# Performance work log

Measured on AMD Instinct MI355X. Metric: run time of the kernel, lower is better.

The kernel has to match this reference:

```python
import jax, jax.numpy as jnp
import numpy as np

IN_FEATURES = 256
OUT_FEATURES = 256
INTERNAL = (IN_FEATURES + OUT_FEATURES) // 2  # trajectron AdditiveAttention default


def setup_inputs() -> dict:
    key = jax.random.key(0)
    k1, k2, k3, k4, k5 = jax.random.split(key, 5)
    B, TH, TQ = 32, 256, 64
    inputs = jax.random.normal(k1, (B, TH, IN_FEATURES), dtype=jnp.float32)
    state = jax.random.normal(k2, (B, TQ, OUT_FEATURES), dtype=jnp.float32)
    # Linear weights (no bias), Kaiming-ish scale
    w1 = jax.random.normal(k3, (INTERNAL, IN_FEATURES), dtype=jnp.float32) / np.sqrt(IN_FEATURES)
    w2 = jax.random.normal(k4, (INTERNAL, OUT_FEATURES), dtype=jnp.float32) / np.sqrt(OUT_FEATURES)
    v = jax.random.normal(k5, (INTERNAL,), dtype=jnp.float32) / np.sqrt(INTERNAL)
    return {"inputs": inputs, "state": state, "w1": w1, "w2": w2, "v": v, "batch_size": B}


def reference(inputs, state, w1, w2, v, batch_size):
    # history annotations: (B, Th, Din); future annotations (queries): (B, Tq, Dout)
    keys = inputs.reshape(batch_size, -1, IN_FEATURES)
    queries = state.reshape(batch_size, -1, OUT_FEATURES)
    # Additive (Bahdanau) attention: score = v . tanh(W1 k + W2 q)
    k_proj = jnp.einsum('bti,di->btd', keys, w1)       # (B, Th, D)
    q_proj = jnp.einsum('bqo,do->bqd', queries, w2)    # (B, Tq, D)
    scores = jnp.einsum('d,bqtd->bqt', v, jnp.tanh(q_proj[:, :, None, :] + k_proj[:, None, :, :]))
    alpha = jax.nn.softmax(scores, axis=-1)            # softmax over history axis
    contexts = jnp.einsum('bqt,bti->bqi', alpha, keys)  # (B, Tq, Din)
    # reshape + dropout (eval mode / p effectively 0 -> identity)
    return contexts.reshape(-1, IN_FEATURES)
```

## Files before the change

### kernel.cpp

```cpp
#include <hip/hip_runtime.h>
#include <math.h>

#define BATCH 32
#define TH    256
#define TQn   64
#define DIN   256
#define DD    256
#define QT    4
#define E2C   2.885390081777927f
#define NL2E  -2.8853900817779268f

typedef __attribute__((ext_vector_type(8)))  short bf16x8;
typedef __attribute__((ext_vector_type(16))) float floatx16;
typedef __attribute__((ext_vector_type(4)))  float f32x4;
typedef __attribute__((ext_vector_type(2)))  float f32x2;

__device__ __forceinline__ float eclamp(float x) {
    return __builtin_amdgcn_exp2f(fminf(x * E2C, 15.f));
}

__device__ __forceinline__ f32x2 pk_fma_s(f32x2 a, f32x2 b, f32x2 c) {
    f32x2 d;
    asm("v_pk_fma_f32 %0, %1, %2, %3" : "=v"(d) : "s"(a), "v"(b), "v"(c));
    return d;
}
__device__ __forceinline__ f32x2 pk_mul_s(f32x2 a, f32x2 b) {
    f32x2 d;
    asm("v_pk_mul_f32 %0, %1, %2" : "=v"(d) : "s"(a), "v"(b));
    return d;
}
__device__ __forceinline__ f32x2 pk_mul_v(f32x2 a, f32x2 b) {
    f32x2 d;
    asm("v_pk_mul_f32 %0, %1, %2" : "=v"(d) : "v"(a), "v"(b));
    return d;
}

__device__ __forceinline__ unsigned cvt_pk_bf16(float x0, float x1) {
    unsigned r;
    asm("v_cvt_pk_bf16_f32 %0, %1, %2" : "=v"(r) : "v"(x0), "v"(x1));
    return r;
}
__device__ __forceinline__ void split2(float x0, float x1, unsigned& hi, unsigned& lo) {
    unsigned h = cvt_pk_bf16(x0, x1);
    float f0 = __uint_as_float(h << 16);
    float f1 = __uint_as_float(h & 0xFFFF0000u);
    hi = h;
    lo = cvt_pk_bf16(x0 - f0, x1 - f1);
}

__device__ __forceinline__ void split8(float4 f0, float4 f1, uint4& hi, uint4& lo) {
    split2(f0.x, f0.y, hi.x, lo.x);
    split2(f0.z, f0.w, hi.y, lo.y);
    split2(f1.x, f1.y, hi.z, lo.z);
    split2(f1.z, f1.w, hi.w, lo.w);
}

#define REG4  65
#define WOFF  (16 * REG4)
#define TSTR  68
__global__ __launch_bounds__(256, 4)
void proj_kernel(const float* __restrict__ keys,
                 const float* __restrict__ state,
                 const float* __restrict__ w1,
                 const float* __restrict__ w2,
                 const float* __restrict__ vvec,
                 float* __restrict__ ktp,
                 float* __restrict__ qpo,
                 float* __restrict__ vperm)
{
    __shared__ uint4 lds4[2 * 16 * REG4];

    const int bid = blockIdx.x;
    const int tid = threadIdx.x;

    const int xcd  = bid & 7;
    const int slot = bid >> 3;
    const int bb   = xcd + 8 * (slot / 20);
    const int j    = slot % 20;

    const float* X;
    const float* W;
    int m0, n0;
    bool is_kp;
    if (j < 16) {
        is_kp = true;
        m0 = bb * 256 + (j >> 2) * 64;
        n0 = (j & 3) * 64;
        X = keys; W = w1;
    } else {
        is_kp = false;
        m0 = bb * 64;
        n0 = (j - 16) * 64;
        X = state; W = w2;
    }

    const int w    = tid >> 6;
    const int l    = tid & 63;
    const int mt   = w >> 1;
    const int nt   = w & 1;
    const int srow = tid >> 3;
    const int kg   = tid & 7;
    const int s_s  = kg >> 1;
    const int lidx = (srow & 31) + 32 * (kg & 1);

    floatx16 acc = {};

    #pragma unroll
    for (int k0 = 0; k0 < DIN; k0 += 64) {
        #pragma unroll
        for (int hrow = 0; hrow < 2; hrow++) {
            int m = srow + hrow * 32;
            const float* px = X + (size_t)(m0 + m) * DIN + k0 + kg * 8;
            uint4 hi, lo;
            split8(*(const float4*)px, *(const float4*)(px + 4), hi, lo);
            int g = m >> 5;
            lds4[((0 * 2 + g) * 4 + s_s) * REG4 + lidx] = hi;
            lds4[((2 + g) * 4 + s_s) * REG4 + lidx] = lo;
            const float* pw = W + (size_t)(n0 + m) * DIN + k0 + kg * 8;
            split8(*(const float4*)pw, *(const float4*)(pw + 4), hi, lo);
            lds4[WOFF + ((0 * 2 + g) * 4 + s_s) * REG4 + lidx] = hi;
            lds4[WOFF + ((2 + g) * 4 + s_s) * REG4 + lidx] = lo;
        }
        __syncthreads();

        #pragma unroll
        for (int s = 0; s < 4; s++) {
            uint4 ahr = lds4[((0 * 2 + mt) * 4 + s) * REG4 + l];
            uint4 alr = lds4[((2 + mt) * 4 + s) * REG4 + l];
            uint4 bhr = lds4[WOFF + ((0 * 2 + nt) * 4 + s) * REG4 + l];
            uint4 blr = lds4[WOFF + ((2 + nt) * 4 + s) * REG4 + l];
            bf16x8 ah = __builtin_bit_cast(bf16x8, ahr);
            bf16x8 al = __builtin_bit_cast(bf16x8, alr);
            bf16x8 bh = __builtin_bit_cast(bf16x8, bhr);
            bf16x8 bl = __builtin_bit_cast(bf16x8, blr);
            acc = __builtin_amdgcn_mfma_f32_32x32x16_bf16(ah, bh, acc, 0, 0, 0);
            acc = __builtin_amdgcn_mfma_f32_32x32x16_bf16(al, bh, acc, 0, 0, 0);
            acc = __builtin_amdgcn_mfma_f32_32x32x16_bf16(ah, bl, acc, 0, 0, 0);
        }
        __syncthreads();
    }

    const int col = l & 31;
    const int hl  = l >> 5;
    if (is_kp) {
        float* sT = (float*)lds4;
        const int d_local = nt * 32 + col;
        #pragma unroll
        for (int r = 0; r < 16; r++) {
            int t_local = mt * 32 + 4 * hl + 8 * (r >> 2) + (r & 3);
            sT[t_local * TSTR + d_local] = eclamp(acc[r]);
        }
        __syncthreads();
        const int b  = m0 >> 8;
        const int t0 = m0 & 255;
        float4* dst4 = (float4*)ktp;
        #pragma unroll
        for (int p = 0; p < 4; p++) {
            int dp_local = w * 4 + p;
            float4 v4 = *(float4*)&sT[l * TSTR + dp_local * 4];
            float4 w4;
            w4.x = v4.x; w4.y = v4.z; w4.z = v4.y; w4.w = v4.w;
            dst4[(size_t)(b * 64 + (n0 >> 2) + dp_local) * 256 + t0 + l] = w4;
        }
    } else {
        const int d  = n0 + nt * 32 + col;
        const int dl = d & 3;
        const int dsd = (d & ~3) | ((dl & 1) << 1) | (dl >> 1);
        #pragma unroll
        for (int r = 0; r < 16; r++) {
            int row = (r & 3) + 8 * (r >> 2) + 4 * hl;
            qpo[(size_t)(m0 + mt * 32 + row) * DD + dsd] = eclamp(acc[r]);
        }
        if (!is_kp && bb == 0 && n0 == 0 && tid < 256) {
            int jl = tid & 3;
            vperm[tid] = vvec[(tid & ~3) | ((jl & 1) << 1) | (jl >> 1)];
        }
    }
}

__global__ __launch_bounds__(1024, 8)
void attn_kernel(const float* __restrict__ keys,
                 const float* __restrict__ vvec,
                 const float* __restrict__ ktp,
                 const float* __restrict__ qp,
                 float* __restrict__ out)
{
    __shared__ float s_part[4][QT][TH];
    __shared__ float s_alpha[QT][TH];
    __shared__ float s_rsum[QT];

    const int bid  = blockIdx.x;
    const int b    = bid & 31;
    const int q0   = (bid >> 5) * QT;
    const int tid  = threadIdx.x;
    const int t    = tid & 255;
    const int dgu  = __builtin_amdgcn_readfirstlane(tid >> 8);
    const int lane = tid & 63;
    const int wv   = tid >> 6;

    float acc[QT];
    #pragma unroll
    for (int q = 0; q < QT; q++) acc[q] = 0.f;

    const float4* kb4 = (const float4*)ktp + ((size_t)(b * 64 + dgu * 16) * 256 + t);
    const float* pqr0 = qp + (size_t)(b * TQn + q0 + 0) * DD + dgu * 64;
    const float* pqr1 = qp + (size_t)(b * TQn + q0 + 1) * DD + dgu * 64;
    const float* pqr2 = qp + (size_t)(b * TQn + q0 + 2) * DD + dgu * 64;
    const float* pqr3 = qp + (size_t)(b * TQn + q0 + 3) * DD + dgu * 64;
    const float* vvp  = vvec + dgu * 64;

    const f32x2 one2 = {1.f, 1.f};

    float4 kv0 = kb4[0 * 256], kv1 = kb4[1 * 256],
           kv2 = kb4[2 * 256], kv3 = kb4[3 * 256];

    #pragma unroll
    for (int c = 0; c < 4; c++) {
        float4 n0v, n1v, n2v, n3v;
        if (c < 3) {
            const float4* p = kb4 + (size_t)(c + 1) * 4 * 256;
            n0v = p[0 * 256]; n1v = p[1 * 256];
            n2v = p[2 * 256]; n3v = p[3 * 256];
        }
        #pragma unroll
        for (int u = 0; u < 4; u++) {
            const int dp = c * 4 + u;
            float4 kv = (u == 0) ? kv0 : (u == 1) ? kv1 : (u == 2) ? kv2 : kv3;
            f32x2 KA = {kv.x, kv.y};
            f32x2 KB = {kv.z, kv.w};
            f32x4 V4 = *(const f32x4*)(vvp + dp * 4);
            f32x2 VA = {V4[0], V4[1]};
            f32x2 VB = {V4[2], V4[3]};
            const float* pqr[QT] = {pqr0, pqr1, pqr2, pqr3};
            #pragma unroll
            for (int q = 0; q < QT; q++) {
                const float* pr = pqr[q];
                f32x4 P4 = *(const f32x4*)(pr + dp * 4);
                f32x2 PA = {P4[0], P4[1]};
                f32x2 PB = {P4[2], P4[3]};
                f32x2 A = pk_fma_s(PA, KA, one2);
                f32x2 B = pk_fma_s(PB, KB, one2);
                f32x2 D = pk_mul_v(A, B);
                f32x2 T = pk_mul_s(VA, B);
                f32x2 N = pk_fma_s(VB, A, T);
                float num = fmaf(N[1], D[0], N[0] * D[1]);
                float den = D[0] * D[1];
                acc[q] = fmaf(num, __builtin_amdgcn_rcpf(den), acc[q]);
            }
        }
        if (c < 3) { kv0 = n0v; kv1 = n1v; kv2 = n2v; kv3 = n3v; }
    }

    #pragma unroll
    for (int q = 0; q < QT; q++) s_part[dgu][q][t] = acc[q];
    __syncthreads();

    if (wv < QT) {
        const int q = wv;
        float p0 = s_part[0][q][lane]       + s_part[1][q][lane]
                 + s_part[2][q][lane]       + s_part[3][q][lane];
        float p1 = s_part[0][q][lane + 64]  + s_part[1][q][lane + 64]
                 + s_part[2][q][lane + 64]  + s_part[3][q][lane + 64];
        float p2 = s_part[0][q][lane + 128] + s_part[1][q][lane + 128]
                 + s_part[2][q][lane + 128] + s_part[3][q][lane + 128];
        float p3 = s_part[0][q][lane + 192] + s_part[1][q][lane + 192]
                 + s_part[2][q][lane + 192] + s_part[3][q][lane + 192];
        float e0 = __builtin_amdgcn_exp2f(p0 * NL2E);
        float e1 = __builtin_amdgcn_exp2f(p1 * NL2E);
        float e2 = __builtin_amdgcn_exp2f(p2 * NL2E);
        float e3 = __builtin_amdgcn_exp2f(p3 * NL2E);
        s_alpha[q][lane]       = e0;
        s_alpha[q][lane + 64]  = e1;
        s_alpha[q][lane + 128] = e2;
        s_alpha[q][lane + 192] = e3;
        float s = (e0 + e1) + (e2 + e3);
        #pragma unroll
        for (int off = 32; off >= 1; off >>= 1) s += __shfl_xor(s, off);
        if (lane == 0) s_rsum[q] = 1.f / s;
    }
    __syncthreads();

    {
        const int iqg = __builtin_amdgcn_readfirstlane((tid >> 6) & 3);
        const int il  = lane & 15;
        const int tl  = lane >> 4;
        const int iq  = iqg * 16 + il;

        f32x4 ctx4[QT] = {};
        const float* kp0 = keys + ((size_t)b * TH + dgu * 64 + tl) * DIN + iq * 4;

        #pragma unroll 4
        for (int step = 0; step < 16; step++) {
            f32x4 key4 = *(const f32x4*)(kp0 + (size_t)step * 4 * DIN);
            const int ta = dgu * 64 + step * 4 + tl;
            #pragma unroll
            for (int q = 0; q < QT; q++)
                ctx4[q] += key4 * s_alpha[q][ta];
        }

        #pragma unroll
        for (int q = 0; q < QT; q++) {
            #pragma unroll
            for (int k = 0; k < 4; k++) {
                ctx4[q][k] += __shfl_xor(ctx4[q][k], 16);
                ctx4[q][k] += __shfl_xor(ctx4[q][k], 32);
            }
        }
        if (tl == 0) {
            #pragma unroll
            for (int q = 0; q < QT; q++)
                *(f32x4*)&s_part[dgu][q][iq * 4] = ctx4[q];
        }
    }
    __syncthreads();

    if (tid < 256) {
        const int q = tid >> 6, iqf = tid & 63;
        f32x4 s = *(const f32x4*)&s_part[0][q][iqf * 4];
        s += *(const f32x4*)&s_part[1][q][iqf * 4];
        s += *(const f32x4*)&s_part[2][q][iqf * 4];
        s += *(const f32x4*)&s_part[3][q][iqf * 4];
        s *= s_rsum[q];
        *(f32x4*)&out[(size_t)(b * TQn + q0 + q) * DIN + iqf * 4] = s;
    }
}

extern "C" void kernel_launch(void* const* d_in, const int* in_sizes, int n_in,
                              void* d_out, int out_size, void* d_ws, size_t ws_size,
                              hipStream_t stream) {
    (void)in_sizes; (void)n_in; (void)out_size; (void)ws_size;
    const float* keys  = (const float*)d_in[0];
    const float* state = (const float*)d_in[1];
    const float* w1    = (const float*)d_in[2];
    const float* w2    = (const float*)d_in[3];
    const float* v     = (const float*)d_in[4];
    float* out = (float*)d_out;

    float* ktp = (float*)d_ws;
    float* qp  = ktp + (size_t)BATCH * DD * TH;
    float* vp  = qp + (size_t)BATCH * TQn * DD;

    hipLaunchKernelGGL(proj_kernel, dim3(640), dim3(256), 0, stream,
                       keys, state, w1, w2, v, ktp, qp, vp);
    hipLaunchKernelGGL(attn_kernel, dim3(BATCH * (TQn / QT)), dim3(1024), 0, stream,
                       keys, vp, ktp, qp, out);
}
```

Before: 99.45 us.

## Fuse projection and attention into one cooperative kernel with grid sync

```diff
diff --git a/kernel.cpp b/kernel.cpp
--- a/kernel.cpp
+++ b/kernel.cpp
@@ -1,5 +1,8 @@
 #include <hip/hip_runtime.h>
+#include <hip/hip_cooperative_groups.h>
 #include <math.h>
+
+namespace cg = cooperative_groups;
 
 #define BATCH 32
 #define TH    256
@@ -55,51 +58,21 @@
     split2(f1.z, f1.w, hi.w, lo.w);
 }
 
-#define REG4  65
+#define REG4  64
 #define WOFF  (16 * REG4)
 #define TSTR  68
-__global__ __launch_bounds__(256, 4)
-void proj_kernel(const float* __restrict__ keys,
-                 const float* __restrict__ state,
-                 const float* __restrict__ w1,
-                 const float* __restrict__ w2,
-                 const float* __restrict__ vvec,
-                 float* __restrict__ ktp,
-                 float* __restrict__ qpo,
-                 float* __restrict__ vperm)
+__device__ __forceinline__ void proj_tile(
+    const float* __restrict__ X, const float* __restrict__ W,
+    int m0, int n0, bool is_kp,
+    uint4* __restrict__ lds4, int gt,
+    float* __restrict__ ktp, float* __restrict__ qpo)
 {
-    __shared__ uint4 lds4[2 * 16 * REG4];
-
-    const int bid = blockIdx.x;
-    const int tid = threadIdx.x;
-
-    const int xcd  = bid & 7;
-    const int slot = bid >> 3;
-    const int bb   = xcd + 8 * (slot / 20);
-    const int j    = slot % 20;
-
-    const float* X;
-    const float* W;
-    int m0, n0;
-    bool is_kp;
-    if (j < 16) {
-        is_kp = true;
-        m0 = bb * 256 + (j >> 2) * 64;
-        n0 = (j & 3) * 64;
-        X = keys; W = w1;
-    } else {
-        is_kp = false;
-        m0 = bb * 64;
-        n0 = (j - 16) * 64;
-        X = state; W = w2;
-    }
-
-    const int w    = tid >> 6;
-    const int l    = tid & 63;
+    const int w    = gt >> 6;
+    const int l    = gt & 63;
     const int mt   = w >> 1;
     const int nt   = w & 1;
-    const int srow = tid >> 3;
-    const int kg   = tid & 7;
+    const int srow = gt >> 3;
+    const int kg   = gt & 7;
     const int s_s  = kg >> 1;
     const int lidx = (srow & 31) + 32 * (kg & 1);
 
@@ -163,6 +136,7 @@
             dst4[(size_t)(b * 64 + (n0 >> 2) + dp_local) * 256 + t0 + l] = w4;
         }
     } else {
+        __syncthreads();
         const int d  = n0 + nt * 32 + col;
         const int dl = d & 3;
         const int dsd = (d & ~3) | ((dl & 1) << 1) | (dl >> 1);
@@ -171,28 +145,18 @@
             int row = (r & 3) + 8 * (r >> 2) + 4 * hl;
             qpo[(size_t)(m0 + mt * 32 + row) * DD + dsd] = eclamp(acc[r]);
         }
-        if (!is_kp && bb == 0 && n0 == 0 && tid < 256) {
-            int jl = tid & 3;
-            vperm[tid] = vvec[(tid & ~3) | ((jl & 1) << 1) | (jl >> 1)];
-        }
-    }
-}
-
-__global__ __launch_bounds__(1024, 8)
-void attn_kernel(const float* __restrict__ keys,
-                 const float* __restrict__ vvec,
-                 const float* __restrict__ ktp,
-                 const float* __restrict__ qp,
-                 float* __restrict__ out)
+    }
+}
+
+__device__ __forceinline__ void attn_body(
+    int bid, int tid,
+    const float* __restrict__ keys, const float* __restrict__ vvec,
+    const float* __restrict__ ktp, const float* __restrict__ qp,
+    float* __restrict__ out,
+    float* __restrict__ sp, float* __restrict__ sa, float* __restrict__ sr)
 {
-    __shared__ float s_part[4][QT][TH];
-    __shared__ float s_alpha[QT][TH];
-    __shared__ float s_rsum[QT];
-
-    const int bid  = blockIdx.x;
     const int b    = bid & 31;
     const int q0   = (bid >> 5) * QT;
-    const int tid  = threadIdx.x;
     const int t    = tid & 255;
     const int dgu  = __builtin_amdgcn_readfirstlane(tid >> 8);
     const int lane = tid & 63;
@@ -252,31 +216,31 @@
     }
 
     #pragma unroll
-    for (int q = 0; q < QT; q++) s_part[dgu][q][t] = acc[q];
+    for (int q = 0; q < QT; q++) sp[(dgu * QT + q) * TH + t] = acc[q];
     __syncthreads();
 
     if (wv < QT) {
         const int q = wv;
-        float p0 = s_part[0][q][lane]       + s_part[1][q][lane]
-                 + s_part[2][q][lane]       + s_part[3][q][lane];
-        float p1 = s_part[0][q][lane + 64]  + s_part[1][q][lane + 64]
-                 + s_part[2][q][lane + 64]  + s_part[3][q][lane + 64];
-        float p2 = s_part[0][q][lane + 128] + s_part[1][q][lane + 128]
-                 + s_part[2][q][lane + 128] + s_part[3][q][lane + 128];
-        float p3 = s_part[0][q][lane + 192] + s_part[1][q][lane + 192]
-                 + s_part[2][q][lane + 192] + s_part[3][q][lane + 192];
+        float p0 = sp[(0 * QT + q) * TH + lane]       + sp[(1 * QT + q) * TH + lane]
+                 + sp[(2 * QT + q) * TH + lane]       + sp[(3 * QT + q) * TH + lane];
+        float p1 = sp[(0 * QT + q) * TH + lane + 64]  + sp[(1 * QT + q) * TH + lane + 64]
+                 + sp[(2 * QT + q) * TH + lane + 64]  + sp[(3 * QT + q) * TH + lane + 64];
+        float p2 = sp[(0 * QT + q) * TH + lane + 128] + sp[(1 * QT + q) * TH + lane + 128]
+                 + sp[(2 * QT + q) * TH + lane + 128] + sp[(3 * QT + q) * TH + lane + 128];
+        float p3 = sp[(0 * QT + q) * TH + lane + 192] + sp[(1 * QT + q) * TH + lane + 192]
+                 + sp[(2 * QT + q) * TH + lane + 192] + sp[(3 * QT + q) * TH + lane + 192];
         float e0 = __builtin_amdgcn_exp2f(p0 * NL2E);
         float e1 = __builtin_amdgcn_exp2f(p1 * NL2E);
         float e2 = __builtin_amdgcn_exp2f(p2 * NL2E);
         float e3 = __builtin_amdgcn_exp2f(p3 * NL2E);
-        s_alpha[q][lane]       = e0;
-        s_alpha[q][lane + 64]  = e1;
-        s_alpha[q][lane + 128] = e2;
-        s_alpha[q][lane + 192] = e3;
+        sa[q * TH + lane]       = e0;
+        sa[q * TH + lane + 64]  = e1;
+        sa[q * TH + lane + 128] = e2;
+        sa[q * TH + lane + 192] = e3;
         float s = (e0 + e1) + (e2 + e3);
         #pragma unroll
         for (int off = 32; off >= 1; off >>= 1) s += __shfl_xor(s, off);
-        if (lane == 0) s_rsum[q] = 1.f / s;
+        if (lane == 0) sr[q] = 1.f / s;
     }
     __syncthreads();
 
@@ -295,7 +259,7 @@
             const int ta = dgu * 64 + step * 4 + tl;
             #pragma unroll
             for (int q = 0; q < QT; q++)
-                ctx4[q] += key4 * s_alpha[q][ta];
+                ctx4[q] += key4 * sa[q * TH + ta];
         }
 
         #pragma unroll
@@ -309,20 +273,112 @@
         if (tl == 0) {
             #pragma unroll
             for (int q = 0; q < QT; q++)
-                *(f32x4*)&s_part[dgu][q][iq * 4] = ctx4[q];
+                *(f32x4*)&sp[(dgu * QT + q) * TH + iq * 4] = ctx4[q];
         }
     }
     __syncthreads();
 
     if (tid < 256) {
         const int q = tid >> 6, iqf = tid & 63;
-        f32x4 s = *(const f32x4*)&s_part[0][q][iqf * 4];
-        s += *(const f32x4*)&s_part[1][q][iqf * 4];
-        s += *(const f32x4*)&s_part[2][q][iqf * 4];
-        s += *(const f32x4*)&s_part[3][q][iqf * 4];
-        s *= s_rsum[q];
+        f32x4 s = *(const f32x4*)&sp[(0 * QT + q) * TH + iqf * 4];
+        s += *(const f32x4*)&sp[(1 * QT + q) * TH + iqf * 4];
+        s += *(const f32x4*)&sp[(2 * QT + q) * TH + iqf * 4];
+        s += *(const f32x4*)&sp[(3 * QT + q) * TH + iqf * 4];
+        s *= sr[q];
         *(f32x4*)&out[(size_t)(b * TQn + q0 + q) * DIN + iqf * 4] = s;
     }
+}
+
+__global__ __launch_bounds__(1024, 8)
+void fused_kernel(const float* __restrict__ keys,
+                  const float* __restrict__ state,
+                  const float* __restrict__ w1,
+                  const float* __restrict__ w2,
+                  const float* __restrict__ vvec,
+                  float* __restrict__ ktp,
+                  float* __restrict__ qpo,
+                  float* __restrict__ vperm,
+                  float* __restrict__ out)
+{
+    __shared__ uint4 smem4[4096];
+
+    const int bid = blockIdx.x;
+    const int tid = threadIdx.x;
+    const int grp = tid >> 8;
+    const int gt  = tid & 255;
+    const int xcd = bid & 7;
+    const int s   = bid >> 3;
+
+    if (grp == 0) {
+        const int bb = xcd + 8 * (s >> 4);
+        const int jk = s & 15;
+        proj_tile(keys, w1, bb * 256 + (jk >> 2) * 64, (jk & 3) * 64, true,
+                  smem4, gt, ktp, qpo);
+    } else if (grp == 1 && s < 16) {
+        const int bb = xcd + 8 * (s >> 2);
+        proj_tile(state, w2, bb * 64, (s & 3) * 64, false,
+                  smem4 + 2048, gt, ktp, qpo);
+        if (bid == 0) {
+            int jl = gt & 3;
+            vperm[gt] = vvec[(gt & ~3) | ((jl & 1) << 1) | (jl >> 1)];
+        }
+    } else {
+        #pragma unroll 1
+        for (int i = 0; i < 9; ++i) __syncthreads();
+    }
+
+    __threadfence();
+    cg::this_grid().sync();
+
+    float* fbase = (float*)smem4;
+    attn_body(bid, tid, keys, vperm, ktp, qpo, out,
+              fbase, fbase + 4 * QT * TH, fbase + 5 * QT * TH);
+}
+
+__global__ __launch_bounds__(256, 4)
+void proj_kernel(const float* __restrict__ keys,
+                 const float* __restrict__ state,
+                 const float* __restrict__ w1,
+                 const float* __restrict__ w2,
+                 const float* __restrict__ vvec,
+                 float* __restrict__ ktp,
+                 float* __restrict__ qpo,
+                 float* __restrict__ vperm)
+{
+    __shared__ uint4 lds4[2048];
+
+    const int bid = blockIdx.x;
+    const int tid = threadIdx.x;
+
+    const int xcd  = bid & 7;
+    const int slot = bid >> 3;
+    const int bb   = xcd + 8 * (slot / 20);
+    const int j    = slot % 20;
+
+    if (j < 16) {
+        proj_tile(keys, w1, bb * 256 + (j >> 2) * 64, (j & 3) * 64, true,
+                  lds4, tid, ktp, qpo);
+    } else {
+        proj_tile(state, w2, bb * 64, (j - 16) * 64, false,
+                  lds4, tid, ktp, qpo);
+        if (bb == 0 && j == 16 && tid < 256) {
+            int jl = tid & 3;
+            vperm[tid] = vvec[(tid & ~3) | ((jl & 1) << 1) | (jl >> 1)];
+        }
+    }
+}
+
+__global__ __launch_bounds__(1024, 8)
+void attn_kernel(const float* __restrict__ keys,
+                 const float* __restrict__ vvec,
+                 const float* __restrict__ ktp,
+                 const float* __restrict__ qp,
+                 float* __restrict__ out)
+{
+    __shared__ float sp[4 * QT * TH];
+    __shared__ float sa[QT * TH];
+    __shared__ float sr[QT];
+    attn_body(blockIdx.x, threadIdx.x, keys, vvec, ktp, qp, out, sp, sa, sr);
 }
 
 extern "C" void kernel_launch(void* const* d_in, const int* in_sizes, int n_in,
@@ -340,8 +396,16 @@
     float* qp  = ktp + (size_t)BATCH * DD * TH;
     float* vp  = qp + (size_t)BATCH * TQn * DD;
 
-    hipLaunchKernelGGL(proj_kernel, dim3(640), dim3(256), 0, stream,
-                       keys, state, w1, w2, v, ktp, qp, vp);
-    hipLaunchKernelGGL(attn_kernel, dim3(BATCH * (TQn / QT)), dim3(1024), 0, stream,
-                       keys, vp, ktp, qp, out);
-}
+    void* kargs[] = {(void*)&keys, (void*)&state, (void*)&w1, (void*)&w2,
+                     (void*)&v, (void*)&ktp, (void*)&qp, (void*)&vp, (void*)&out};
+    hipError_t err = hipLaunchCooperativeKernel((const void*)fused_kernel,
+                                                dim3(512), dim3(1024),
+                                                kargs, 0, stream);
+    if (err != hipSuccess) {
+        (void)hipGetLastError();
+        hipLaunchKernelGGL(proj_kernel, dim3(640), dim3(256), 0, stream,
+                           keys, state, w1, w2, v, ktp, qp, vp);
+        hipLaunchKernelGGL(attn_kernel, dim3(BATCH * (TQn / QT)), dim3(1024), 0, stream,
+                           keys, vp, ktp, qp, out);
+    }
+}
```

After: 362.1 us. 264% more time.
